# Kernel tuning notes

Measured on AMD Instinct MI355X. Metric: run time of the kernel, lower is better.

## Reference

```python
import jax, jax.numpy as jnp
import numpy as np

T, B, I, H = 512, 64, 128, 1024


def setup_inputs() -> dict:
    key = jax.random.key(0)
    k1, k2, k3, k4 = jax.random.split(key, 4)
    # scale recurrent weights to keep tanh in a reasonable regime (spectral-radius-ish)
    return {
        "x": jax.random.normal(k1, (T, B, I), dtype=jnp.float32),
        "h0": jnp.zeros((B, H), dtype=jnp.float32),
        "w_ih": jax.random.normal(k2, (H, I), dtype=jnp.float32) / np.sqrt(I),
        "w_hh": jax.random.normal(k3, (H, H), dtype=jnp.float32) * (0.9 / np.sqrt(H)),
        "b": jax.random.normal(k4, (H,), dtype=jnp.float32) * 0.1,
    }


def reference(x, h0, w_ih, w_hh, b):
    # ESNLayer: python loop over time -> lax.scan with the recurrent carry.
    # cell: h_t = tanh(x_t @ W_ih^T + h_{t-1} @ W_hh^T + b); out_t = h_t
    def step(h, x_t):
        h_new = jnp.tanh(x_t @ w_ih.T + h @ w_hh.T + b)  # [B, H]
        return h_new, h_new

    h_final, outputs = jax.lax.scan(step, h0, x)  # outputs: [T, B, H]
    return outputs, h_final
```

## Files before the change

### kernel.cpp

```cpp
#include <hip/hip_runtime.h>
#include <math.h>


#define T_STEPS 512
#define BATCH   64
#define HDIM    1024
#define IDIM    128
#define KDIM    1152
#define NWG     256
#define NB      8

typedef float f32x4_t __attribute__((ext_vector_type(4)));

__device__ __forceinline__ unsigned sc_load(const unsigned* p) {
    unsigned v;
    asm volatile("global_load_dword %0, %1, off sc0 sc1\n\ts_waitcnt vmcnt(0)"
                 : "=&v"(v) : "v"(p) : "memory");
    return v;
}

__device__ __forceinline__ void sc_load4x4(const float* p0, const float* p1,
                                           const float* p2, const float* p3,
                                           float4& a, float4& b,
                                           float4& c, float4& d) {
    asm volatile(
        "global_load_dwordx4 %0, %4, off sc0 sc1\n\t"
        "global_load_dwordx4 %1, %5, off sc0 sc1\n\t"
        "global_load_dwordx4 %2, %6, off sc0 sc1\n\t"
        "global_load_dwordx4 %3, %7, off sc0 sc1\n\t"
        "s_waitcnt vmcnt(0)"
        : "=&v"(a), "=&v"(b), "=&v"(c), "=&v"(d)
        : "v"(p0), "v"(p1), "v"(p2), "v"(p3)
        : "memory");
}

__device__ __forceinline__ void sc_store4(float* p, float4 v) {
    f32x4_t t;
    t.x = v.x; t.y = v.y; t.z = v.z; t.w = v.w;
    asm volatile("global_store_dwordx4 %0, %1, off sc0 sc1\n\ts_waitcnt vmcnt(0)"
                 :: "v"(p), "v"(t) : "memory");
}

__device__ __forceinline__ void flag_store(unsigned* p, unsigned v) {
    asm volatile("global_store_dword %0, %1, off sc0 sc1"
                 :: "v"(p), "v"(v) : "memory");
}

__device__ __forceinline__ void group_barrier(unsigned* flags, int wg, int bgrp,
                                              int tid, unsigned tgt) {
    __syncthreads();
    if (tid == 0)
        flag_store(&flags[wg * 32], tgt);
    if (tid < 32)
        while (sc_load(&flags[(bgrp * 32 + tid) * 32]) < tgt) {}
    __syncthreads();
}

__global__ void transpose_f32(const float* __restrict__ src, float* __restrict__ dst,
                              int R, int C) {
    __shared__ float tile[64][65];
    const int tcol = threadIdx.x & 63;
    const int trow = threadIdx.x >> 6;
    const int nbx = C >> 6;
    const int bx = blockIdx.x % nbx;
    const int by = blockIdx.x / nbx;
    const int c0 = bx << 6, r0 = by << 6;
    for (int i = trow; i < 64; i += 4)
        tile[i][tcol] = src[(size_t)(r0 + i) * C + c0 + tcol];
    __syncthreads();
    for (int i = trow; i < 64; i += 4)
        dst[(size_t)(c0 + i) * R + r0 + tcol] = tile[tcol][i];
}

__global__ __launch_bounds__(512) void esn_persistent(
    const float* __restrict__ x,
    const float* __restrict__ h0,
    const float* __restrict__ WT,
    const float* __restrict__ bias,
    float* __restrict__ out,
    float* __restrict__ hfin,
    unsigned* flags)
{
    const int tid  = threadIdx.x;
    const int wg   = blockIdx.x;
    const int wave = tid >> 6;
    const int lane = tid & 63;
    const int jq   = lane & 7;
    const int ksub = lane >> 3;
    const int jblk = ((wg & 7) << 2) | ((wg >> 3) & 3);
    const int bgrp = wg >> 5;
    const int b0   = bgrp << 3;
    const int j0   = (jblk << 5) + (jq << 2);
    const int krec = wave << 7;
    const int kx   = HDIM + (wave << 4) + (ksub << 1);

    __shared__ float  ht[NB][KDIM];
    __shared__ float4 red[8 * 8 * 9];

    float4 Wv[18];
    {
        const float* wp = WT + (size_t)krec * HDIM + j0;
        #pragma unroll
        for (int i = 0; i < 4; ++i) {
            const int kk = ((i << 3) + ksub) << 2;
            const float* wk = wp + (size_t)kk * HDIM;
            Wv[i * 4 + 0] = *(const float4*)(wk);
            Wv[i * 4 + 1] = *(const float4*)(wk + HDIM);
            Wv[i * 4 + 2] = *(const float4*)(wk + 2 * HDIM);
            Wv[i * 4 + 3] = *(const float4*)(wk + 3 * HDIM);
        }
        const float* wkx = WT + (size_t)kx * HDIM + j0;
        Wv[16] = *(const float4*)(wkx);
        Wv[17] = *(const float4*)(wkx + HDIM);
    }

    float4 b4 = make_float4(0.f, 0.f, 0.f, 0.f);
    int jj = 0, bb_ep = 0;
    if (tid < 64) {
        bb_ep = tid >> 3;
        jj = (jblk << 5) + ((tid & 7) << 2);
        b4 = *(const float4*)(bias + jj);
    }

    float4 xv = make_float4(0.f, 0.f, 0.f, 0.f);
    if (lane < 32)
        xv = *(const float4*)(x + (size_t)(b0 + wave) * IDIM + (lane << 2));

    for (int t = 0; t < T_STEPS; ++t) {
        const float* hrow = t ? (out + ((size_t)(t - 1) * BATCH + b0 + wave) * HDIM)
                              : (h0 + (size_t)(b0 + wave) * HDIM);
        {
            float4 a, b, c, d;
            const float* p = hrow + (lane << 2);
            sc_load4x4(p, p + 256, p + 512, p + 768, a, b, c, d);
            *(float4*)&ht[wave][(lane << 2)]       = a;
            *(float4*)&ht[wave][256 + (lane << 2)] = b;
            *(float4*)&ht[wave][512 + (lane << 2)] = c;
            *(float4*)&ht[wave][768 + (lane << 2)] = d;
        }
        if (lane < 32)
            *(float4*)&ht[wave][HDIM + (lane << 2)] = xv;
        __syncthreads();

        if (t + 1 < T_STEPS && lane < 32)
            xv = *(const float4*)(x + ((size_t)(t + 1) * BATCH + b0 + wave) * IDIM
                                  + (lane << 2));

        float4 acc[NB];
        #pragma unroll
        for (int bb = 0; bb < NB; ++bb) acc[bb] = make_float4(0.f, 0.f, 0.f, 0.f);

        #pragma unroll
        for (int i = 0; i < 4; ++i) {
            const int kk = krec + ((((i << 3) + ksub)) << 2);
            const float4 w0 = Wv[i * 4 + 0], w1 = Wv[i * 4 + 1];
            const float4 w2 = Wv[i * 4 + 2], w3 = Wv[i * 4 + 3];
            #pragma unroll
            for (int bb = 0; bb < NB; ++bb) {
                float4 h4 = *(const float4*)&ht[bb][kk];
                acc[bb].x = fmaf(w0.x, h4.x, acc[bb].x);
                acc[bb].y = fmaf(w0.y, h4.x, acc[bb].y);
                acc[bb].z = fmaf(w0.z, h4.x, acc[bb].z);
                acc[bb].w = fmaf(w0.w, h4.x, acc[bb].w);
                acc[bb].x = fmaf(w1.x, h4.y, acc[bb].x);
                acc[bb].y = fmaf(w1.y, h4.y, acc[bb].y);
                acc[bb].z = fmaf(w1.z, h4.y, acc[bb].z);
                acc[bb].w = fmaf(w1.w, h4.y, acc[bb].w);
                acc[bb].x = fmaf(w2.x, h4.z, acc[bb].x);
                acc[bb].y = fmaf(w2.y, h4.z, acc[bb].y);
                acc[bb].z = fmaf(w2.z, h4.z, acc[bb].z);
                acc[bb].w = fmaf(w2.w, h4.z, acc[bb].w);
                acc[bb].x = fmaf(w3.x, h4.w, acc[bb].x);
                acc[bb].y = fmaf(w3.y, h4.w, acc[bb].y);
                acc[bb].z = fmaf(w3.z, h4.w, acc[bb].z);
                acc[bb].w = fmaf(w3.w, h4.w, acc[bb].w);
            }
        }
        #pragma unroll
        for (int bb = 0; bb < NB; ++bb) {
            float2 hx = *(const float2*)&ht[bb][kx];
            acc[bb].x = fmaf(Wv[16].x, hx.x, acc[bb].x);
            acc[bb].y = fmaf(Wv[16].y, hx.x, acc[bb].y);
            acc[bb].z = fmaf(Wv[16].z, hx.x, acc[bb].z);
            acc[bb].w = fmaf(Wv[16].w, hx.x, acc[bb].w);
            acc[bb].x = fmaf(Wv[17].x, hx.y, acc[bb].x);
            acc[bb].y = fmaf(Wv[17].y, hx.y, acc[bb].y);
            acc[bb].z = fmaf(Wv[17].z, hx.y, acc[bb].z);
            acc[bb].w = fmaf(Wv[17].w, hx.y, acc[bb].w);
        }

        #pragma unroll
        for (int bb = 0; bb < NB; ++bb) {
            acc[bb].x += __shfl_xor(acc[bb].x, 8);
            acc[bb].y += __shfl_xor(acc[bb].y, 8);
            acc[bb].z += __shfl_xor(acc[bb].z, 8);
            acc[bb].w += __shfl_xor(acc[bb].w, 8);
            acc[bb].x += __shfl_xor(acc[bb].x, 16);
            acc[bb].y += __shfl_xor(acc[bb].y, 16);
            acc[bb].z += __shfl_xor(acc[bb].z, 16);
            acc[bb].w += __shfl_xor(acc[bb].w, 16);
            acc[bb].x += __shfl_xor(acc[bb].x, 32);
            acc[bb].y += __shfl_xor(acc[bb].y, 32);
            acc[bb].z += __shfl_xor(acc[bb].z, 32);
            acc[bb].w += __shfl_xor(acc[bb].w, 32);
        }
        if (ksub == 0) {
            #pragma unroll
            for (int bb = 0; bb < NB; ++bb)
                red[((wave << 3) + jq) * 9 + bb] = acc[bb];
        }
        __syncthreads();

        if (tid < 64) {
            float4 s = make_float4(0.f, 0.f, 0.f, 0.f);
            #pragma unroll
            for (int w = 0; w < 8; ++w) {
                float4 r = red[((w << 3) + (tid & 7)) * 9 + bb_ep];
                s.x += r.x; s.y += r.y; s.z += r.z; s.w += r.w;
            }
            float4 o;
            o.x = tanhf(s.x + b4.x);
            o.y = tanhf(s.y + b4.y);
            o.z = tanhf(s.z + b4.z);
            o.w = tanhf(s.w + b4.w);
            sc_store4(out + ((size_t)t * BATCH + b0 + bb_ep) * HDIM + jj, o);
            if (t == T_STEPS - 1)
                *(float4*)(hfin + (size_t)(b0 + bb_ep) * HDIM + jj) = o;
        }

        if (t != T_STEPS - 1)
            group_barrier(flags, wg, bgrp, tid, (unsigned)(t + 1));
    }
}

extern "C" void kernel_launch(void* const* d_in, const int* in_sizes, int n_in,
                              void* d_out, int out_size, void* d_ws, size_t ws_size,
                              hipStream_t stream) {
    const float* x    = (const float*)d_in[0];
    const float* h0   = (const float*)d_in[1];
    const float* w_ih = (const float*)d_in[2];
    const float* w_hh = (const float*)d_in[3];
    const float* bias = (const float*)d_in[4];
    float* out = (float*)d_out;

    char* ws = (char*)d_ws;
    float*    WT    = (float*)ws;
    unsigned* flags = (unsigned*)(ws + 4718592);

    (void)hipMemsetAsync(flags, 0, 32768, stream);
    transpose_f32<<<256, 256, 0, stream>>>(w_hh, WT, HDIM, HDIM);
    transpose_f32<<<32, 256, 0, stream>>>(w_ih, WT + (size_t)HDIM * HDIM, HDIM, IDIM);
    esn_persistent<<<NWG, 512, 0, stream>>>(x, h0, WT, bias,
                                            out, out + (size_t)T_STEPS * BATCH * HDIM,
                                            flags);
}
```

Measured before the change: 3.125 ms.

## Replace group barrier with per-wave fine-grained flags and local reuse of own output

Drops the per-step group barrier across workgroups. Each wave now polls a per-row, per-producer flag right before loading only the h slice it needs. Each workgroup writes its own new h chunk straight into shared memory and skips reloading it from global. The epilogue moves to the first 8 lanes of every wave, and each wave's lane 0 publishes its own flag. Loads become contiguous 64-byte chunks per lane. The aim is to cut the barrier's latency and serialization, at the risk of subtle memory-ordering bugs between the flag store and the data store.

New measurement: 3.523 ms. +12.7%, slower.

```diff
diff --git a/kernel.cpp b/kernel.cpp
--- a/kernel.cpp
+++ b/kernel.cpp
@@ -19,18 +19,16 @@
     return v;
 }
 
-__device__ __forceinline__ void sc_load4x4(const float* p0, const float* p1,
-                                           const float* p2, const float* p3,
-                                           float4& a, float4& b,
-                                           float4& c, float4& d) {
+__device__ __forceinline__ void sc_load64(const float* p, float4& a, float4& b,
+                                          float4& c, float4& d) {
     asm volatile(
         "global_load_dwordx4 %0, %4, off sc0 sc1\n\t"
-        "global_load_dwordx4 %1, %5, off sc0 sc1\n\t"
-        "global_load_dwordx4 %2, %6, off sc0 sc1\n\t"
-        "global_load_dwordx4 %3, %7, off sc0 sc1\n\t"
+        "global_load_dwordx4 %1, %4, off offset:16 sc0 sc1\n\t"
+        "global_load_dwordx4 %2, %4, off offset:32 sc0 sc1\n\t"
+        "global_load_dwordx4 %3, %4, off offset:48 sc0 sc1\n\t"
         "s_waitcnt vmcnt(0)"
         : "=&v"(a), "=&v"(b), "=&v"(c), "=&v"(d)
-        : "v"(p0), "v"(p1), "v"(p2), "v"(p3)
+        : "v"(p)
         : "memory");
 }
 
@@ -44,16 +42,6 @@
 __device__ __forceinline__ void flag_store(unsigned* p, unsigned v) {
     asm volatile("global_store_dword %0, %1, off sc0 sc1"
                  :: "v"(p), "v"(v) : "memory");
-}
-
-__device__ __forceinline__ void group_barrier(unsigned* flags, int wg, int bgrp,
-                                              int tid, unsigned tgt) {
-    __syncthreads();
-    if (tid == 0)
-        flag_store(&flags[wg * 32], tgt);
-    if (tid < 32)
-        while (sc_load(&flags[(bgrp * 32 + tid) * 32]) < tgt) {}
-    __syncthreads();
 }
 
 __global__ void transpose_f32(const float* __restrict__ src, float* __restrict__ dst,
@@ -115,31 +103,43 @@
     }
 
     float4 b4 = make_float4(0.f, 0.f, 0.f, 0.f);
-    int jj = 0, bb_ep = 0;
-    if (tid < 64) {
-        bb_ep = tid >> 3;
-        jj = (jblk << 5) + ((tid & 7) << 2);
+    int jj = 0;
+    if (lane < 8) {
+        jj = (jblk << 5) + (lane << 2);
         b4 = *(const float4*)(bias + jj);
     }
+
+    const bool own = ((lane >> 1) == jblk);
+
+    unsigned* fl_base = flags + (((bgrp << 3) + wave) << 5);
+    const unsigned* fl_poll = fl_base + (lane >> 1);
 
     float4 xv = make_float4(0.f, 0.f, 0.f, 0.f);
     if (lane < 32)
         xv = *(const float4*)(x + (size_t)(b0 + wave) * IDIM + (lane << 2));
 
     for (int t = 0; t < T_STEPS; ++t) {
-        const float* hrow = t ? (out + ((size_t)(t - 1) * BATCH + b0 + wave) * HDIM)
-                              : (h0 + (size_t)(b0 + wave) * HDIM);
-        {
-            float4 a, b, c, d;
-            const float* p = hrow + (lane << 2);
-            sc_load4x4(p, p + 256, p + 512, p + 768, a, b, c, d);
-            *(float4*)&ht[wave][(lane << 2)]       = a;
-            *(float4*)&ht[wave][256 + (lane << 2)] = b;
-            *(float4*)&ht[wave][512 + (lane << 2)] = c;
-            *(float4*)&ht[wave][768 + (lane << 2)] = d;
-        }
         if (lane < 32)
             *(float4*)&ht[wave][HDIM + (lane << 2)] = xv;
+        if (t == 0) {
+            float4 a, b, c, d;
+            const float* p = h0 + (size_t)(b0 + wave) * HDIM + (lane << 4);
+            sc_load64(p, a, b, c, d);
+            *(float4*)&ht[wave][(lane << 4) + 0]  = a;
+            *(float4*)&ht[wave][(lane << 4) + 4]  = b;
+            *(float4*)&ht[wave][(lane << 4) + 8]  = c;
+            *(float4*)&ht[wave][(lane << 4) + 12] = d;
+        } else if (!own) {
+            while (sc_load(fl_poll) < (unsigned)t) {}
+            float4 a, b, c, d;
+            const float* p = out + ((size_t)(t - 1) * BATCH + b0 + wave) * HDIM
+                             + (lane << 4);
+            sc_load64(p, a, b, c, d);
+            *(float4*)&ht[wave][(lane << 4) + 0]  = a;
+            *(float4*)&ht[wave][(lane << 4) + 4]  = b;
+            *(float4*)&ht[wave][(lane << 4) + 8]  = c;
+            *(float4*)&ht[wave][(lane << 4) + 12] = d;
+        }
         __syncthreads();
 
         if (t + 1 < T_STEPS && lane < 32)
@@ -211,11 +211,11 @@
         }
         __syncthreads();
 
-        if (tid < 64) {
+        if (lane < 8) {
             float4 s = make_float4(0.f, 0.f, 0.f, 0.f);
             #pragma unroll
             for (int w = 0; w < 8; ++w) {
-                float4 r = red[((w << 3) + (tid & 7)) * 9 + bb_ep];
+                float4 r = red[((w << 3) + lane) * 9 + wave];
                 s.x += r.x; s.y += r.y; s.z += r.z; s.w += r.w;
             }
             float4 o;
@@ -223,13 +223,13 @@
             o.y = tanhf(s.y + b4.y);
             o.z = tanhf(s.z + b4.z);
             o.w = tanhf(s.w + b4.w);
-            sc_store4(out + ((size_t)t * BATCH + b0 + bb_ep) * HDIM + jj, o);
+            *(float4*)&ht[wave][(jblk << 5) + (lane << 2)] = o;
+            sc_store4(out + ((size_t)t * BATCH + b0 + wave) * HDIM + jj, o);
             if (t == T_STEPS - 1)
-                *(float4*)(hfin + (size_t)(b0 + bb_ep) * HDIM + jj) = o;
-        }
-
-        if (t != T_STEPS - 1)
-            group_barrier(flags, wg, bgrp, tid, (unsigned)(t + 1));
+                *(float4*)(hfin + (size_t)(b0 + wave) * HDIM + jj) = o;
+        }
+        if (lane == 0)
+            flag_store(fl_base + jblk, (unsigned)(t + 1));
     }
 }
 
@@ -247,7 +247,7 @@
     float*    WT    = (float*)ws;
     unsigned* flags = (unsigned*)(ws + 4718592);
 
-    (void)hipMemsetAsync(flags, 0, 32768, stream);
+    (void)hipMemsetAsync(flags, 0, 8192, stream);
     transpose_f32<<<256, 256, 0, stream>>>(w_hh, WT, HDIM, HDIM);
     transpose_f32<<<32, 256, 0, stream>>>(w_ih, WT + (size_t)HDIM * HDIM, HDIM, IDIM);
     esn_persistent<<<NWG, 512, 0, stream>>>(x, h0, WT, bias,
```
